# Optimization experiments

Hardware: AMD Instinct MI355X
Metric: run time of the kernel (lower is better)

Reference implementation:

```python
import jax, jax.numpy as jnp
import numpy as np

B, C, H, W = 2, 512, 64, 64
NUM_GROUPS = 32
EPS = 1e-6


def setup_inputs() -> dict:
    key = jax.random.key(0)
    ks = jax.random.split(key, 6)
    s = 1.0 / np.sqrt(C)
    return {
        "x": jax.random.normal(ks[0], (B, C, H, W), dtype=jnp.float32),
        "gn_scale": jnp.ones((C,), jnp.float32),
        "gn_bias": jnp.zeros((C,), jnp.float32),
        "wq": jax.random.normal(ks[1], (C, C), jnp.float32) * s,
        "bq": jnp.zeros((C,), jnp.float32),
        "wk": jax.random.normal(ks[2], (C, C), jnp.float32) * s,
        "bk": jnp.zeros((C,), jnp.float32),
        "wv": jax.random.normal(ks[3], (C, C), jnp.float32) * s,
        "bv": jnp.zeros((C,), jnp.float32),
        "wp": jax.random.normal(ks[4], (C, C), jnp.float32) * s,
        "bp": jnp.zeros((C,), jnp.float32),
    }


def group_norm(x, scale, bias):
    # x: [b, c, h, w]; GroupNorm with NUM_GROUPS groups, eps=1e-6, affine
    b, c, h, w = x.shape
    xg = x.reshape(b, NUM_GROUPS, c // NUM_GROUPS, h, w)
    mean = jnp.mean(xg, axis=(2, 3, 4), keepdims=True)
    var = jnp.var(xg, axis=(2, 3, 4), keepdims=True)
    xg = (xg - mean) * jax.lax.rsqrt(var + EPS)
    xn = xg.reshape(b, c, h, w)
    return xn * scale[None, :, None, None] + bias[None, :, None, None]


def reference(x, gn_scale, gn_bias, wq, bq, wk, bk, wv, bv, wp, bp):
    b, c, h, w = x.shape
    n = h * w
    hn = group_norm(x, gn_scale, gn_bias).reshape(b, c, n)  # [b,c,n]
    # 1x1 convs == per-pixel linear over channels
    q = jnp.einsum('dc,bcn->bdn', wq, hn) + bq[None, :, None]
    k = jnp.einsum('dc,bcn->bdn', wk, hn) + bk[None, :, None]
    v = jnp.einsum('dc,bcn->bdn', wv, hn) + bv[None, :, None]
    # attn[b,i,j] = softmax_j( q[:, :, i] . k[:, :, j] / sqrt(c) )
    attn = jnp.einsum('bci,bcj->bij', q, k) * (float(c) ** -0.5)
    attn = jax.nn.softmax(attn, axis=-1)
    out = jnp.einsum('bcj,bij->bci', v, attn)  # [b,c,n]
    out = jnp.einsum('dc,bcn->bdn', wp, out) + bp[None, :, None]
    return x + out.reshape(b, c, h, w)
```

## Files before the change

### kernel.cpp

```cpp
#include <hip/hip_runtime.h>

typedef __bf16 bf16x8 __attribute__((ext_vector_type(8)));
typedef float f32x4 __attribute__((ext_vector_type(4)));
typedef int i32x8 __attribute__((ext_vector_type(8)));


#if defined(__has_builtin)
#if __has_builtin(__builtin_amdgcn_global_load_lds)
#define HAS_GLL 1
#endif
#endif

__device__ __forceinline__ void async_copy16(const void* g, void* l) {
#ifdef HAS_GLL
    __builtin_amdgcn_global_load_lds(
        (const __attribute__((address_space(1))) unsigned int*)g,
        (__attribute__((address_space(3))) unsigned int*)l, 16, 0, 0);
#else
    *(int4*)l = *(const int4*)g;
#endif
}

__device__ __forceinline__ unsigned char to_fp8(float v) {
    return (unsigned char)(__builtin_amdgcn_cvt_pk_fp8_f32(v, v, 0, false) & 0xFF);
}

#define MXSCALE 0x7F7F7F7F

#define ASM_VMCNT(N) asm volatile("s_waitcnt vmcnt(" #N ")" ::: "memory")
#define ASM_LGKM0() asm volatile("s_waitcnt lgkmcnt(0)" ::: "memory")

__global__ __launch_bounds__(256) void prep_kernel(
    const float* __restrict__ x, float* __restrict__ ps,
    const float* __restrict__ wq, const float* __restrict__ wk,
    const float* __restrict__ wv, const float* __restrict__ wp,
    const float* __restrict__ bq, const float* __restrict__ bk,
    unsigned char* __restrict__ wqk8, unsigned char* __restrict__ wv8,
    __bf16* __restrict__ wp_b, float* __restrict__ bqk) {
    if (blockIdx.x >= 1024) {
        int idx = (blockIdx.x - 1024) * 256 + threadIdx.x;
        wqk8[idx] = to_fp8(wq[idx]);
        wqk8[262144 + idx] = to_fp8(wk[idx]);
        wv8[idx] = to_fp8(wv[idx]);
        wp_b[idx] = (__bf16)wp[idx];
        if (idx < 512) {
            bqk[idx] = bq[idx];
            bqk[512 + idx] = bk[idx];
        }
        return;
    }
    int blk = blockIdx.x;
    const float4* base = (const float4*)x + (size_t)blk * 1024;
    float s1 = 0.f, s2 = 0.f;
#pragma unroll
    for (int i = 0; i < 4; ++i) {
        float4 v = base[threadIdx.x + (i << 8)];
        s1 += v.x + v.y + v.z + v.w;
        s2 += v.x * v.x + v.y * v.y + v.z * v.z + v.w * v.w;
    }
    for (int off = 32; off >= 1; off >>= 1) {
        s1 += __shfl_xor(s1, off);
        s2 += __shfl_xor(s2, off);
    }
    __shared__ float r1[4], r2[4];
    int wave = threadIdx.x >> 6, lane = threadIdx.x & 63;
    if (lane == 0) { r1[wave] = s1; r2[wave] = s2; }
    __syncthreads();
    if (threadIdx.x == 0) {
        ps[blk] = r1[0] + r1[1] + r1[2] + r1[3];
        ps[1024 + blk] = r2[0] + r2[1] + r2[2] + r2[3];
    }
}

__global__ __launch_bounds__(256) void gn_apply_kernel(const float* __restrict__ x,
                                                       const float* __restrict__ gn_scale,
                                                       const float* __restrict__ gn_bias,
                                                       const float* __restrict__ ps,
                                                       unsigned char* __restrict__ hn8) {
    __shared__ float tile[32][33];
    int b = blockIdx.z;
    int n0 = blockIdx.x * 32, c0 = blockIdx.y * 32;
    int tx = threadIdx.x & 31, ty = threadIdx.x >> 5;
    const float* xb = x + (size_t)b * 512 * 4096;
#pragma unroll
    for (int r = 0; r < 4; ++r) {
        int c = ty + r * 8;
        tile[c][tx] = xb[(size_t)(c0 + c) * 4096 + n0 + tx];
    }
    int c = c0 + tx;
    int g = (b << 5) + (c >> 4);
    float s1 = 0.f, s2 = 0.f;
#pragma unroll
    for (int i = 0; i < 16; ++i) {
        s1 += ps[(g << 4) + i];
        s2 += ps[1024 + (g << 4) + i];
    }
    float m = s1 * (1.f / 65536.f);
    float var = s2 * (1.f / 65536.f) - m * m;
    float rs = rsqrtf(var + 1e-6f);
    float sc = gn_scale[c] * rs;
    float bi = gn_bias[c] - m * sc;
    __syncthreads();
    unsigned char* outp = hn8 + (size_t)b * 4096 * 512;
#pragma unroll
    for (int r = 0; r < 4; ++r) {
        int n = ty + r * 8;
        float v = tile[tx][n];
        outp[(size_t)(n0 + n) * 512 + c] = to_fp8(v * sc + bi);
    }
}

template <int BN, int OUT_MODE, int BIAS_MODE>
__device__ __forceinline__ void mx_gemm_body(
    const unsigned char* __restrict__ Ab, int lda,
    const unsigned char* __restrict__ Bb, int ldb,
    void* __restrict__ C, int ldc,
    const float* __restrict__ bias, int K, float scale,
    long m0, long n0, unsigned char* As, unsigned char* Bs) {
    constexpr int NT = BN / 32;
    const int tid = threadIdx.x;
    const int lane = tid & 63, wave = tid >> 6;
    const int ln = lane & 15, q = lane >> 4;
    const int wm = (wave >> 1) << 6;
    const int wn = (wave & 1) * (BN / 2);

    f32x4 acc[4][NT] = {};

    const int nk = K >> 7;
    for (int ki = 0; ki < nk; ++ki) {
        const int k0 = ki << 7;
        __syncthreads();
#pragma unroll
        for (int p = 0; p < 4; ++p) {
            int c = (p << 8) + tid;
            int row = c >> 3, sg = ((c & 7) ^ (row & 7)) << 4;
            async_copy16(Ab + (long)row * lda + k0 + sg, &As[c << 4]);
        }
#pragma unroll
        for (int p = 0; p < NT; ++p) {
            int c = (p << 8) + tid;
            int row = c >> 3, sg = ((c & 7) ^ (row & 7)) << 4;
            async_copy16(Bb + (long)row * ldb + k0 + sg, &Bs[c << 4]);
        }
        __syncthreads();
        i32x8 af[4], bf[NT];
#pragma unroll
        for (int t = 0; t < 4; ++t) {
            int row = wm + t * 16 + ln, e = row & 7;
            const unsigned char* ap = &As[row << 7];
            *(int4*)&af[t] = *(const int4*)(ap + ((((q << 1)) ^ e) << 4));
            *((int4*)&af[t] + 1) = *(const int4*)(ap + ((((q << 1) | 1) ^ e) << 4));
        }
#pragma unroll
        for (int t = 0; t < NT; ++t) {
            int row = wn + t * 16 + ln, e = row & 7;
            const unsigned char* bp = &Bs[row << 7];
            *(int4*)&bf[t] = *(const int4*)(bp + ((((q << 1)) ^ e) << 4));
            *((int4*)&bf[t] + 1) = *(const int4*)(bp + ((((q << 1) | 1) ^ e) << 4));
        }
        __builtin_amdgcn_s_setprio(1);
#pragma unroll
        for (int mt = 0; mt < 4; ++mt)
#pragma unroll
            for (int nt = 0; nt < NT; ++nt)
                acc[mt][nt] = __builtin_amdgcn_mfma_scale_f32_16x16x128_f8f6f4(
                    af[mt], bf[nt], acc[mt][nt], 0, 0, 0, MXSCALE, 0, MXSCALE);
        __builtin_amdgcn_s_setprio(0);
    }

#pragma unroll
    for (int mt = 0; mt < 4; ++mt) {
#pragma unroll
        for (int nt = 0; nt < NT; ++nt) {
            long col = n0 + wn + nt * 16 + ln;
#pragma unroll
            for (int r = 0; r < 4; ++r) {
                long row = m0 + wm + mt * 16 + (q << 2) + r;
                float v = acc[mt][nt][r] * scale;
                if (BIAS_MODE == 1) v += bias[row];
                if (BIAS_MODE == 2) v += bias[col];
                long off = row * (long)ldc + col;
                if (OUT_MODE == 0) {
                    ((unsigned char*)C)[off] = to_fp8(v);
                } else if (OUT_MODE == 1) {
                    ((_Float16*)C)[off] = (_Float16)v;
                } else {
                    ((__bf16*)C)[off] = (__bf16)v;
                }
            }
        }
    }
}

__global__ __launch_bounds__(256) void qkv_kernel(
    const unsigned char* __restrict__ hn8, const unsigned char* __restrict__ wqk8,
    const unsigned char* __restrict__ wv8, const float* __restrict__ bqk,
    const float* __restrict__ bv, unsigned char* __restrict__ qk8,
    unsigned char* __restrict__ v8) {
    __shared__ __align__(16) unsigned char As[128 * 128];
    __shared__ __align__(16) unsigned char Bs[128 * 128];
    int z = blockIdx.z;
    if (z < 2) {
        long b = z;
        long m0 = (long)blockIdx.y * 128, n0 = (long)blockIdx.x * 128;
        mx_gemm_body<128, 0, 2>(hn8 + b * 4096 * 512 + m0 * 512, 512,
                                wqk8 + n0 * 512, 512,
                                qk8 + b * 4096 * 1024, 1024,
                                bqk, 512, 1.f, m0, n0, As, Bs);
    } else {
        long b = z - 2;
        int flat = blockIdx.y * 8 + blockIdx.x;
        long m0 = (long)(flat >> 6) * 128, n0 = (long)(flat & 63) * 64;
        mx_gemm_body<64, 0, 1>(wv8 + m0 * 512, 512,
                               hn8 + b * 4096 * 512 + n0 * 512, 512,
                               v8 + b * 512 * 4096, 4096,
                               bv, 512, 1.f, m0, n0, As, Bs);
    }
}

__global__ __launch_bounds__(256) void mx_s_softmax_kernel(
    const unsigned char* __restrict__ QK, unsigned char* __restrict__ P8,
    float* __restrict__ pmaxF, float* __restrict__ psumF, float scale) {
    __shared__ __align__(16) unsigned char As[128 * 128];
    __shared__ __align__(16) unsigned char Bs[128 * 128];
    __shared__ float sm_max[2][128], sm_sum[2][128];
    int id = (blockIdx.x & 7) * 256 + (blockIdx.x >> 3);
    int mg = id >> 5;
    long b = mg >> 5;
    int panel = mg & 31;
    long j0 = (long)panel * 128;
    long i0 = (long)(id & 31) * 128;
    const unsigned char* Ab = QK + b * 4096 * 1024 + j0 * 1024 + 512;
    const unsigned char* Bb = QK + b * 4096 * 1024 + i0 * 1024;

    const int tid = threadIdx.x;
    const int lane = tid & 63, wave = tid >> 6;
    const int ln = lane & 15, q = lane >> 4;
    const int wm = (wave >> 1) << 6;
    const int wn = (wave & 1) * 64;

    f32x4 acc[4][4] = {};

    for (int ki = 0; ki < 4; ++ki) {
        const int k0 = ki << 7;
        __syncthreads();
#pragma unroll
        for (int p = 0; p < 4; ++p) {
            int c = (p << 8) + tid;
            int row = c >> 3, sg = ((c & 7) ^ (row & 7)) << 4;
            async_copy16(Ab + (long)row * 1024 + k0 + sg, &As[c << 4]);
        }
#pragma unroll
        for (int p = 0; p < 4; ++p) {
            int c = (p << 8) + tid;
            int row = c >> 3, sg = ((c & 7) ^ (row & 7)) << 4;
            async_copy16(Bb + (long)row * 1024 + k0 + sg, &Bs[c << 4]);
        }
        __syncthreads();
        i32x8 af[4], bf[4];
#pragma unroll
        for (int t = 0; t < 4; ++t) {
            int row = wm + t * 16 + ln, e = row & 7;
            const unsigned char* ap = &As[row << 7];
            *(int4*)&af[t] = *(const int4*)(ap + ((((q << 1)) ^ e) << 4));
            *((int4*)&af[t] + 1) = *(const int4*)(ap + ((((q << 1) | 1) ^ e) << 4));
        }
#pragma unroll
        for (int t = 0; t < 4; ++t) {
            int row = wn + t * 16 + ln, e = row & 7;
            const unsigned char* bp = &Bs[row << 7];
            *(int4*)&bf[t] = *(const int4*)(bp + ((((q << 1)) ^ e) << 4));
            *((int4*)&bf[t] + 1) = *(const int4*)(bp + ((((q << 1) | 1) ^ e) << 4));
        }
        __builtin_amdgcn_s_setprio(1);
#pragma unroll
        for (int mt = 0; mt < 4; ++mt)
#pragma unroll
            for (int nt = 0; nt < 4; ++nt)
                acc[mt][nt] = __builtin_amdgcn_mfma_scale_f32_16x16x128_f8f6f4(
                    af[mt], bf[nt], acc[mt][nt], 0, 0, 0, MXSCALE, 0, MXSCALE);
        __builtin_amdgcn_s_setprio(0);
    }

    const float C_ = scale * 1.4426950408889634f;
#pragma unroll
    for (int mt = 0; mt < 4; ++mt)
#pragma unroll
        for (int nt = 0; nt < 4; ++nt)
#pragma unroll
            for (int r = 0; r < 4; ++r) acc[mt][nt][r] *= C_;

#pragma unroll
    for (int nt = 0; nt < 4; ++nt) {
        float m = acc[0][nt][0];
#pragma unroll
        for (int mt = 0; mt < 4; ++mt)
#pragma unroll
            for (int r = 0; r < 4; ++r) m = fmaxf(m, acc[mt][nt][r]);
        m = fmaxf(m, __shfl_xor(m, 16));
        m = fmaxf(m, __shfl_xor(m, 32));
        if (lane < 16) sm_max[wave >> 1][wn + nt * 16 + ln] = m;
    }
    __syncthreads();

    unsigned int* rp = (unsigned int*)As;
    float mtl[4];
#pragma unroll
    for (int nt = 0; nt < 4; ++nt) {
        const int i = wn + nt * 16 + ln;
        mtl[nt] = ceilf(fmaxf(sm_max[0][i], sm_max[1][i]));
        float s = 0.f;
#pragma unroll
        for (int mt = 0; mt < 4; ++mt) {
            float p0 = exp2f(acc[mt][nt][0] - mtl[nt]);
            float p1 = exp2f(acc[mt][nt][1] - mtl[nt]);
            float p2 = exp2f(acc[mt][nt][2] - mtl[nt]);
            float p3 = exp2f(acc[mt][nt][3] - mtl[nt]);
            s += (p0 + p1) + (p2 + p3);
            int w = __builtin_amdgcn_cvt_pk_fp8_f32(p0, p1, 0, false);
            w = __builtin_amdgcn_cvt_pk_fp8_f32(p2, p3, w, true);
            int jq = ((wave >> 1) << 4) + (mt << 2) + q;
            rp[i * 32 + (jq ^ ((i & 7) << 2))] = (unsigned int)w;
        }
        s += __shfl_xor(s, 16);
        s += __shfl_xor(s, 32);
        if (lane < 16) sm_sum[wave >> 1][i] = s;
    }
    __syncthreads();

    if (wave < 2 && lane < 16) {
#pragma unroll
        for (int nt = 0; nt < 4; ++nt) {
            int i = wn + nt * 16 + ln;
            long rowg = b * 4096 + i0 + i;
            pmaxF[rowg * 32 + panel] = mtl[nt];
            psumF[rowg * 32 + panel] = sm_sum[0][i] + sm_sum[1][i];
        }
    }

    {
        const int i = tid >> 1, half = tid & 1;
        const unsigned int* rr = rp + i * 32;
        unsigned char* Pw = P8 + b * 4096 * 4096 + (i0 + i) * 4096 + j0 + half * 64;
#pragma unroll
        for (int k = 0; k < 4; ++k) {
            int js = (half * 16 + 4 * k) ^ ((i & 7) << 2);
            *(int4*)(Pw + k * 16) = *(const int4*)(rr + js);
        }
    }
}

__global__ __launch_bounds__(256) void mx_pv_scaled_kernel(
    const unsigned char* __restrict__ P, const unsigned char* __restrict__ V,
    const float* __restrict__ pmaxF, const float* __restrict__ psumF,
    __bf16* __restrict__ O) {
    __shared__ __align__(16) unsigned char As[2 * 128 * 128];
    __shared__ __align__(16) unsigned char Bs[2 * 64 * 128];
    __shared__ __align__(16) unsigned char sb_lds[128 * 32];
    __shared__ float inv_lds[128];
    const int tid = threadIdx.x;
    const int lane = tid & 63, wave = tid >> 6;
    const int ln = lane & 15, q = lane >> 4;
    const int wm = (wave >> 1) << 6, wn = (wave & 1) << 5;
    const int b = blockIdx.x >> 5;
    const long m0 = (long)(blockIdx.x & 31) * 128;
    const long n0 = (long)blockIdx.y * 64;
    const long rowg0 = (long)b * 4096 + m0;

    if (tid < 128) {
        const float4* pm4 = (const float4*)(pmaxF + (rowg0 + tid) * 32);
        const float4* ps4 = (const float4*)(psumF + (rowg0 + tid) * 32);
        float4 pm[8], ps[8];
#pragma unroll
        for (int i = 0; i < 8; ++i) { pm[i] = pm4[i]; ps[i] = ps4[i]; }
        float g = -1e30f;
#pragma unroll
        for (int i = 0; i < 8; ++i)
            g = fmaxf(g, fmaxf(fmaxf(pm[i].x, pm[i].y), fmaxf(pm[i].z, pm[i].w)));
        float denom = 0.f;
        unsigned int* sbw = (unsigned int*)sb_lds + tid * 8;
#pragma unroll
        for (int i = 0; i < 8; ++i) {
            float d0 = pm[i].x - g, d1 = pm[i].y - g, d2 = pm[i].z - g, d3 = pm[i].w - g;
            denom += ps[i].x * exp2f(d0) + ps[i].y * exp2f(d1) +
                     ps[i].z * exp2f(d2) + ps[i].w * exp2f(d3);
            int b0 = 127 + (int)d0, b1 = 127 + (int)d1, b2 = 127 + (int)d2, b3 = 127 + (int)d3;
            b0 = b0 < 0 ? 0 : b0; b1 = b1 < 0 ? 0 : b1;
            b2 = b2 < 0 ? 0 : b2; b3 = b3 < 0 ? 0 : b3;
            sbw[i] = (unsigned)b0 | ((unsigned)b1 << 8) | ((unsigned)b2 << 16) |
                     ((unsigned)b3 << 24);
        }
        inv_lds[tid] = 1.f / denom;
    }
    __syncthreads();

    const unsigned char* Pb = P + rowg0 * 4096;
    const unsigned char* Vb = V + ((long)b * 512 + n0) * 4096;

    f32x4 acc[4][2] = {};

    auto stage = [&](int kt, int buf) {
        const int k0 = kt << 7;
        unsigned char* Ad = As + buf * 16384;
        unsigned char* Bd = Bs + buf * 8192;
#pragma unroll
        for (int p = 0; p < 4; ++p) {
            int c = (p << 8) + tid;
            int row = c >> 3, sg = ((c & 7) ^ (row & 7)) << 4;
            async_copy16(Pb + (long)row * 4096 + k0 + sg, Ad + (c << 4));
        }
#pragma unroll
        for (int p = 0; p < 2; ++p) {
            int c = (p << 8) + tid;
            int row = c >> 3, sg = ((c & 7) ^ (row & 7)) << 4;
            async_copy16(Vb + (long)row * 4096 + k0 + sg, Bd + (c << 4));
        }
    };

    stage(0, 0);
    stage(1, 1);
    for (int ki = 0; ki < 32; ++ki) {
        if (ki < 31) ASM_VMCNT(6);
        else ASM_VMCNT(0);
        __builtin_amdgcn_s_barrier();
        const int cur = ki & 1;
        const unsigned char* Ar = As + cur * 16384;
        const unsigned char* Br = Bs + cur * 8192;
        i32x8 af[4], bf[2];
        int saw[4];
#pragma unroll
        for (int t = 0; t < 4; ++t) {
            int row = wm + t * 16 + ln, e = row & 7;
            const unsigned char* ap = Ar + (row << 7);
            *(int4*)&af[t] = *(const int4*)(ap + ((((q << 1)) ^ e) << 4));
            *((int4*)&af[t] + 1) = *(const int4*)(ap + ((((q << 1) | 1) ^ e) << 4));
            saw[t] = (int)sb_lds[(row << 5) + ki] * 0x01010101;
        }
#pragma unroll
        for (int t = 0; t < 2; ++t) {
            int row = wn + t * 16 + ln, e = row & 7;
            const unsigned char* bp = Br + (row << 7);
            *(int4*)&bf[t] = *(const int4*)(bp + ((((q << 1)) ^ e) << 4));
            *((int4*)&bf[t] + 1) = *(const int4*)(bp + ((((q << 1) | 1) ^ e) << 4));
        }
        ASM_LGKM0();
        __builtin_amdgcn_s_barrier();
        if (ki + 2 < 32) stage(ki + 2, cur);
        __builtin_amdgcn_s_setprio(1);
#pragma unroll
        for (int mt = 0; mt < 4; ++mt)
#pragma unroll
            for (int nt = 0; nt < 2; ++nt)
                acc[mt][nt] = __builtin_amdgcn_mfma_scale_f32_16x16x128_f8f6f4(
                    af[mt], bf[nt], acc[mt][nt], 0, 0, 0, saw[mt], 0, MXSCALE);
        __builtin_amdgcn_s_setprio(0);
    }

    __bf16* Ob = O + (long)b * 4096 * 512;
#pragma unroll
    for (int mt = 0; mt < 4; ++mt) {
#pragma unroll
        for (int nt = 0; nt < 2; ++nt) {
            long col = n0 + wn + nt * 16 + ln;
#pragma unroll
            for (int r = 0; r < 4; ++r) {
                int rowl = wm + mt * 16 + (q << 2) + r;
                Ob[(m0 + rowl) * 512 + col] = (__bf16)(acc[mt][nt][r] * inv_lds[rowl]);
            }
        }
    }
}

__global__ __launch_bounds__(256) void proj_kernel(
    const __bf16* __restrict__ A, const __bf16* __restrict__ Bt, long bsB,
    float* __restrict__ C, long bsC, const float* __restrict__ bias,
    const float* __restrict__ resid) {
    __shared__ __align__(16) __bf16 As[128][64];
    __shared__ __align__(16) __bf16 Bs[64][64];
    const int tid = threadIdx.x;
    const int wave = tid >> 6, lane = tid & 63;
    const int q = lane >> 4, ln = lane & 15;
    const int wm = wave << 5;
    const long m0 = (long)blockIdx.y * 128, n0 = (long)blockIdx.x * 64;
    const int b = blockIdx.z;
    const __bf16* Ab = A + m0 * 512;
    const __bf16* Bb = Bt + (long)b * bsB + n0 * 512;

    f32x4 acc[2][4] = {};

    for (int k0 = 0; k0 < 512; k0 += 64) {
        __syncthreads();
#pragma unroll
        for (int p = 0; p < 4; ++p) {
            int c = (p << 8) + tid;
            int row = c >> 3, sg = (c & 7) << 3;
            async_copy16(Ab + (long)row * 512 + k0 + sg, &As[0][0] + (c << 3));
        }
#pragma unroll
        for (int p = 0; p < 2; ++p) {
            int c = (p << 8) + tid;
            int row = c >> 3, sg = (c & 7) << 3;
            async_copy16(Bb + (long)row * 512 + k0 + sg, &Bs[0][0] + (c << 3));
        }
        __syncthreads();
#pragma unroll
        for (int kk = 0; kk < 2; ++kk) {
            bf16x8 af[2], bfr[4];
#pragma unroll
            for (int mt = 0; mt < 2; ++mt)
                af[mt] = *(const bf16x8*)(&As[wm + mt * 16 + ln][(kk << 5) + (q << 3)]);
#pragma unroll
            for (int nt = 0; nt < 4; ++nt)
                bfr[nt] = *(const bf16x8*)(&Bs[nt * 16 + ln][(kk << 5) + (q << 3)]);
#pragma unroll
            for (int mt = 0; mt < 2; ++mt)
#pragma unroll
                for (int nt = 0; nt < 4; ++nt)
                    acc[mt][nt] = __builtin_amdgcn_mfma_f32_16x16x32_bf16(
                        af[mt], bfr[nt], acc[mt][nt], 0, 0, 0);
        }
    }

#pragma unroll
    for (int mt = 0; mt < 2; ++mt) {
#pragma unroll
        for (int nt = 0; nt < 4; ++nt) {
            long col = n0 + nt * 16 + ln;
#pragma unroll
            for (int r = 0; r < 4; ++r) {
                long row = m0 + wm + mt * 16 + (q << 2) + r;
                long off = (long)b * bsC + row * 4096 + col;
                C[off] = acc[mt][nt][r] + bias[row] + resid[off];
            }
        }
    }
}

extern "C" void kernel_launch(void* const* d_in, const int* in_sizes, int n_in,
                              void* d_out, int out_size, void* d_ws, size_t ws_size,
                              hipStream_t stream) {
    const float* x = (const float*)d_in[0];
    const float* gn_scale = (const float*)d_in[1];
    const float* gn_bias = (const float*)d_in[2];
    const float* wq = (const float*)d_in[3];
    const float* bq = (const float*)d_in[4];
    const float* wk = (const float*)d_in[5];
    const float* bk = (const float*)d_in[6];
    const float* wv = (const float*)d_in[7];
    const float* bv = (const float*)d_in[8];
    const float* wp = (const float*)d_in[9];
    const float* bp = (const float*)d_in[10];
    float* out = (float*)d_out;

    char* ws = (char*)d_ws;
    unsigned char* wqk8 = (unsigned char*)(ws + 0x0);
    unsigned char* wv8 = (unsigned char*)(ws + 0x80000);
    __bf16* wp_b = (__bf16*)(ws + 0xC0000);
    float* bqk = (float*)(ws + 0x140000);
    float* psum = (float*)(ws + 0x142000);
    unsigned char* hn8 = (unsigned char*)(ws + 0x150000);
    unsigned char* qk8 = (unsigned char*)(ws + 0x550000);
    unsigned char* v8 = (unsigned char*)(ws + 0xD50000);
    __bf16* o_t = (__bf16*)(ws + 0x1150000);
    unsigned char* S8 = (unsigned char*)(ws + 0x1950000);
    float* pmaxF = (float*)(ws + 0x3950000);
    float* psumF = (float*)(ws + 0x3A50000);
    (void)ws_size;

    prep_kernel<<<2048, 256, 0, stream>>>(x, psum, wq, wk, wv, wp, bq, bk,
                                          wqk8, wv8, wp_b, bqk);
    gn_apply_kernel<<<dim3(128, 16, 2), 256, 0, stream>>>(x, gn_scale, gn_bias,
                                                          psum, hn8);
    qkv_kernel<<<dim3(8, 32, 4), 256, 0, stream>>>(hn8, wqk8, wv8, bqk, bv,
                                                   qk8, v8);

    const float attn_scale = 0.044194173824159216f;
    mx_s_softmax_kernel<<<2048, 256, 0, stream>>>(qk8, S8, pmaxF, psumF,
                                                  attn_scale);
    mx_pv_scaled_kernel<<<dim3(64, 8), 256, 0, stream>>>(S8, v8, pmaxF, psumF,
                                                         o_t);

    proj_kernel<<<dim3(64, 4, 2), 256, 0, stream>>>(
        wp_b, o_t, 4096l * 512, out, 512l * 4096, bp, x);
}
```

Baseline: 187.1 us.

## Double-buffer S-softmax GEMM loads and loop four key panels per block

The score/softmax kernel now processes four consecutive 128-wide key panels per block, launching 512 blocks instead of 2048. Its K-loop uses double-buffered LDS with vmcnt-based waits, so global-to-LDS copies overlap the MFMA work. P tiles are now written straight from registers to global memory as 4-byte stores, dropping the LDS staging and swizzled 16-byte write-out. In exchange the kernel uses twice the LDS, which lowers occupancy, and the narrower uncoalesced P stores may waste write bandwidth.

```diff
diff --git a/kernel.cpp b/kernel.cpp
--- a/kernel.cpp
+++ b/kernel.cpp
@@ -221,132 +221,155 @@
 __global__ __launch_bounds__(256) void mx_s_softmax_kernel(
     const unsigned char* __restrict__ QK, unsigned char* __restrict__ P8,
     float* __restrict__ pmaxF, float* __restrict__ psumF, float scale) {
-    __shared__ __align__(16) unsigned char As[128 * 128];
-    __shared__ __align__(16) unsigned char Bs[128 * 128];
+    __shared__ __align__(16) unsigned char As[2 * 128 * 128];
+    __shared__ __align__(16) unsigned char Bs[2 * 128 * 128];
     __shared__ float sm_max[2][128], sm_sum[2][128];
-    int id = (blockIdx.x & 7) * 256 + (blockIdx.x >> 3);
-    int mg = id >> 5;
-    long b = mg >> 5;
-    int panel = mg & 31;
-    long j0 = (long)panel * 128;
-    long i0 = (long)(id & 31) * 128;
-    const unsigned char* Ab = QK + b * 4096 * 1024 + j0 * 1024 + 512;
-    const unsigned char* Bb = QK + b * 4096 * 1024 + i0 * 1024;
+    const int bid = blockIdx.x;
+    const long b = bid >> 8;
+    const int ip = (bid >> 3) & 31, js = bid & 7;
+    const long i0 = (long)ip * 128;
+    const long jb = (long)js * 512;
+    const unsigned char* Qb = QK + b * 4096 * 1024 + i0 * 1024;
+    const unsigned char* Kb = QK + b * 4096 * 1024 + 512;
 
     const int tid = threadIdx.x;
     const int lane = tid & 63, wave = tid >> 6;
     const int ln = lane & 15, q = lane >> 4;
     const int wm = (wave >> 1) << 6;
-    const int wn = (wave & 1) * 64;
-
-    f32x4 acc[4][4] = {};
-
-    for (int ki = 0; ki < 4; ++ki) {
-        const int k0 = ki << 7;
+    const int wn = (wave & 1) << 6;
+    const float C_ = scale * 1.4426950408889634f;
+
+    unsigned char* Pw = P8 + b * 4096 * 4096;
+
+    for (int jp = 0; jp < 4; ++jp) {
+        const long j0 = jb + jp * 128;
+        const int panel = (js << 2) + jp;
+        f32x4 acc[4][4] = {};
+
+#pragma unroll
+        for (int t0 = 0; t0 < 2; ++t0) {
+            const int k0 = t0 << 7;
+            unsigned char* Ad = As + t0 * 16384;
+            unsigned char* Bd = Bs + t0 * 16384;
+#pragma unroll
+            for (int p = 0; p < 4; ++p) {
+                int c = (p << 8) + tid;
+                int row = c >> 3, sg = ((c & 7) ^ (row & 7)) << 4;
+                async_copy16(Kb + (j0 + row) * 1024 + k0 + sg, Ad + (c << 4));
+            }
+#pragma unroll
+            for (int p = 0; p < 4; ++p) {
+                int c = (p << 8) + tid;
+                int row = c >> 3, sg = ((c & 7) ^ (row & 7)) << 4;
+                async_copy16(Qb + (long)row * 1024 + k0 + sg, Bd + (c << 4));
+            }
+        }
+
+        for (int ks = 0; ks < 4; ++ks) {
+            if (ks < 3) ASM_VMCNT(8);
+            else ASM_VMCNT(0);
+            __builtin_amdgcn_s_barrier();
+            const int cur = ks & 1;
+            const unsigned char* Ar = As + cur * 16384;
+            const unsigned char* Br = Bs + cur * 16384;
+            i32x8 af[4], bf[4];
+#pragma unroll
+            for (int t = 0; t < 4; ++t) {
+                int row = wm + t * 16 + ln, e = row & 7;
+                const unsigned char* ap = Ar + (row << 7);
+                *(int4*)&af[t] = *(const int4*)(ap + ((((q << 1)) ^ e) << 4));
+                *((int4*)&af[t] + 1) = *(const int4*)(ap + ((((q << 1) | 1) ^ e) << 4));
+            }
+#pragma unroll
+            for (int t = 0; t < 4; ++t) {
+                int row = wn + t * 16 + ln, e = row & 7;
+                const unsigned char* bp = Br + (row << 7);
+                *(int4*)&bf[t] = *(const int4*)(bp + ((((q << 1)) ^ e) << 4));
+                *((int4*)&bf[t] + 1) = *(const int4*)(bp + ((((q << 1) | 1) ^ e) << 4));
+            }
+            ASM_LGKM0();
+            __builtin_amdgcn_s_barrier();
+            if (ks + 2 < 4) {
+                const int k0 = (ks + 2) << 7;
+                unsigned char* Ad = As + cur * 16384;
+                unsigned char* Bd = Bs + cur * 16384;
+#pragma unroll
+                for (int p = 0; p < 4; ++p) {
+                    int c = (p << 8) + tid;
+                    int row = c >> 3, sg = ((c & 7) ^ (row & 7)) << 4;
+                    async_copy16(Kb + (j0 + row) * 1024 + k0 + sg, Ad + (c << 4));
+                }
+#pragma unroll
+                for (int p = 0; p < 4; ++p) {
+                    int c = (p << 8) + tid;
+                    int row = c >> 3, sg = ((c & 7) ^ (row & 7)) << 4;
+                    async_copy16(Qb + (long)row * 1024 + k0 + sg, Bd + (c << 4));
+                }
+            }
+            __builtin_amdgcn_s_setprio(1);
+#pragma unroll
+            for (int mt = 0; mt < 4; ++mt)
+#pragma unroll
+                for (int nt = 0; nt < 4; ++nt)
+                    acc[mt][nt] = __builtin_amdgcn_mfma_scale_f32_16x16x128_f8f6f4(
+                        af[mt], bf[nt], acc[mt][nt], 0, 0, 0, MXSCALE, 0, MXSCALE);
+            __builtin_amdgcn_s_setprio(0);
+        }
+
+#pragma unroll
+        for (int mt = 0; mt < 4; ++mt)
+#pragma unroll
+            for (int nt = 0; nt < 4; ++nt)
+#pragma unroll
+                for (int r = 0; r < 4; ++r) acc[mt][nt][r] *= C_;
+
+#pragma unroll
+        for (int nt = 0; nt < 4; ++nt) {
+            float m = acc[0][nt][0];
+#pragma unroll
+            for (int mt = 0; mt < 4; ++mt)
+#pragma unroll
+                for (int r = 0; r < 4; ++r) m = fmaxf(m, acc[mt][nt][r]);
+            m = fmaxf(m, __shfl_xor(m, 16));
+            m = fmaxf(m, __shfl_xor(m, 32));
+            if (lane < 16) sm_max[wave >> 1][wn + nt * 16 + ln] = m;
+        }
         __syncthreads();
-#pragma unroll
-        for (int p = 0; p < 4; ++p) {
-            int c = (p << 8) + tid;
-            int row = c >> 3, sg = ((c & 7) ^ (row & 7)) << 4;
-            async_copy16(Ab + (long)row * 1024 + k0 + sg, &As[c << 4]);
-        }
-#pragma unroll
-        for (int p = 0; p < 4; ++p) {
-            int c = (p << 8) + tid;
-            int row = c >> 3, sg = ((c & 7) ^ (row & 7)) << 4;
-            async_copy16(Bb + (long)row * 1024 + k0 + sg, &Bs[c << 4]);
+
+        float mtl[4];
+#pragma unroll
+        for (int nt = 0; nt < 4; ++nt) {
+            const int i = wn + nt * 16 + ln;
+            mtl[nt] = ceilf(fmaxf(sm_max[0][i], sm_max[1][i]));
+            float s = 0.f;
+#pragma unroll
+            for (int mt = 0; mt < 4; ++mt) {
+                float p0 = exp2f(acc[mt][nt][0] - mtl[nt]);
+                float p1 = exp2f(acc[mt][nt][1] - mtl[nt]);
+                float p2 = exp2f(acc[mt][nt][2] - mtl[nt]);
+                float p3 = exp2f(acc[mt][nt][3] - mtl[nt]);
+                s += (p0 + p1) + (p2 + p3);
+                int w = __builtin_amdgcn_cvt_pk_fp8_f32(p0, p1, 0, false);
+                w = __builtin_amdgcn_cvt_pk_fp8_f32(p2, p3, w, true);
+                *(unsigned int*)(Pw + (i0 + i) * 4096 + j0 + wm + mt * 16 + (q << 2)) =
+                    (unsigned int)w;
+            }
+            s += __shfl_xor(s, 16);
+            s += __shfl_xor(s, 32);
+            if (lane < 16) sm_sum[wave >> 1][i] = s;
         }
         __syncthreads();
-        i32x8 af[4], bf[4];
-#pragma unroll
-        for (int t = 0; t < 4; ++t) {
-            int row = wm + t * 16 + ln, e = row & 7;
-            const unsigned char* ap = &As[row << 7];
-            *(int4*)&af[t] = *(const int4*)(ap + ((((q << 1)) ^ e) << 4));
-            *((int4*)&af[t] + 1) = *(const int4*)(ap + ((((q << 1) | 1) ^ e) << 4));
-        }
-#pragma unroll
-        for (int t = 0; t < 4; ++t) {
-            int row = wn + t * 16 + ln, e = row & 7;
-            const unsigned char* bp = &Bs[row << 7];
-            *(int4*)&bf[t] = *(const int4*)(bp + ((((q << 1)) ^ e) << 4));
-            *((int4*)&bf[t] + 1) = *(const int4*)(bp + ((((q << 1) | 1) ^ e) << 4));
-        }
-        __builtin_amdgcn_s_setprio(1);
-#pragma unroll
-        for (int mt = 0; mt < 4; ++mt)
-#pragma unroll
-            for (int nt = 0; nt < 4; ++nt)
-                acc[mt][nt] = __builtin_amdgcn_mfma_scale_f32_16x16x128_f8f6f4(
-                    af[mt], bf[nt], acc[mt][nt], 0, 0, 0, MXSCALE, 0, MXSCALE);
-        __builtin_amdgcn_s_setprio(0);
-    }
-
-    const float C_ = scale * 1.4426950408889634f;
-#pragma unroll
-    for (int mt = 0; mt < 4; ++mt)
-#pragma unroll
-        for (int nt = 0; nt < 4; ++nt)
-#pragma unroll
-            for (int r = 0; r < 4; ++r) acc[mt][nt][r] *= C_;
-
-#pragma unroll
-    for (int nt = 0; nt < 4; ++nt) {
-        float m = acc[0][nt][0];
-#pragma unroll
-        for (int mt = 0; mt < 4; ++mt)
-#pragma unroll
-            for (int r = 0; r < 4; ++r) m = fmaxf(m, acc[mt][nt][r]);
-        m = fmaxf(m, __shfl_xor(m, 16));
-        m = fmaxf(m, __shfl_xor(m, 32));
-        if (lane < 16) sm_max[wave >> 1][wn + nt * 16 + ln] = m;
-    }
-    __syncthreads();
-
-    unsigned int* rp = (unsigned int*)As;
-    float mtl[4];
-#pragma unroll
-    for (int nt = 0; nt < 4; ++nt) {
-        const int i = wn + nt * 16 + ln;
-        mtl[nt] = ceilf(fmaxf(sm_max[0][i], sm_max[1][i]));
-        float s = 0.f;
-#pragma unroll
-        for (int mt = 0; mt < 4; ++mt) {
-            float p0 = exp2f(acc[mt][nt][0] - mtl[nt]);
-            float p1 = exp2f(acc[mt][nt][1] - mtl[nt]);
-            float p2 = exp2f(acc[mt][nt][2] - mtl[nt]);
-            float p3 = exp2f(acc[mt][nt][3] - mtl[nt]);
-            s += (p0 + p1) + (p2 + p3);
-            int w = __builtin_amdgcn_cvt_pk_fp8_f32(p0, p1, 0, false);
-            w = __builtin_amdgcn_cvt_pk_fp8_f32(p2, p3, w, true);
-            int jq = ((wave >> 1) << 4) + (mt << 2) + q;
-            rp[i * 32 + (jq ^ ((i & 7) << 2))] = (unsigned int)w;
-        }
-        s += __shfl_xor(s, 16);
-        s += __shfl_xor(s, 32);
-        if (lane < 16) sm_sum[wave >> 1][i] = s;
-    }
-    __syncthreads();
-
-    if (wave < 2 && lane < 16) {
-#pragma unroll
-        for (int nt = 0; nt < 4; ++nt) {
-            int i = wn + nt * 16 + ln;
-            long rowg = b * 4096 + i0 + i;
-            pmaxF[rowg * 32 + panel] = mtl[nt];
-            psumF[rowg * 32 + panel] = sm_sum[0][i] + sm_sum[1][i];
-        }
-    }
-
-    {
-        const int i = tid >> 1, half = tid & 1;
-        const unsigned int* rr = rp + i * 32;
-        unsigned char* Pw = P8 + b * 4096 * 4096 + (i0 + i) * 4096 + j0 + half * 64;
-#pragma unroll
-        for (int k = 0; k < 4; ++k) {
-            int js = (half * 16 + 4 * k) ^ ((i & 7) << 2);
-            *(int4*)(Pw + k * 16) = *(const int4*)(rr + js);
-        }
+
+        if (wave < 2 && lane < 16) {
+#pragma unroll
+            for (int nt = 0; nt < 4; ++nt) {
+                int i = wn + nt * 16 + ln;
+                long rowg = b * 4096 + i0 + i;
+                pmaxF[rowg * 32 + panel] = mtl[nt];
+                psumF[rowg * 32 + panel] = sm_sum[0][i] + sm_sum[1][i];
+            }
+        }
+        __syncthreads();
     }
 }
 
@@ -575,8 +598,8 @@
                                                    qk8, v8);
 
     const float attn_scale = 0.044194173824159216f;
-    mx_s_softmax_kernel<<<2048, 256, 0, stream>>>(qk8, S8, pmaxF, psumF,
-                                                  attn_scale);
+    mx_s_softmax_kernel<<<512, 256, 0, stream>>>(qk8, S8, pmaxF, psumF,
+                                                 attn_scale);
     mx_pv_scaled_kernel<<<dim3(64, 8), 256, 0, stream>>>(S8, v8, pmaxF, psumF,
                                                          o_t);
 
```

Result: slower. 204.0 us (+9.1%).
